# Kernel tuning notes

Hardware: AMD Instinct MI355X
Metric: run time of the kernel (lower is better)

The kernel has to match this reference:

```python
import jax, jax.numpy as jnp
import numpy as np

D_IN, D_MODEL = 512, 256
B, N = 2, 512


def setup_inputs() -> dict:
    key = jax.random.key(0)
    ks = jax.random.split(key, 8)
    xav_x = float(np.sqrt(2.0 / (D_IN + D_MODEL)))
    xav_p = float(np.sqrt(2.0 / (4 + D_MODEL)))
    return {
        "x": jax.random.normal(ks[0], (B, N, D_IN), dtype=jnp.float32),
        "pos": jax.random.normal(ks[1], (B, N, 4), dtype=jnp.float32),
        "attn_mask": jax.random.randint(ks[2], (B, N, N), 0, 2, dtype=jnp.int32),
        "Wx": jax.random.normal(ks[3], (D_IN, D_MODEL), dtype=jnp.float32) * xav_x,
        "bx": jnp.zeros((D_MODEL,), dtype=jnp.float32),
        "Wp": jax.random.normal(ks[4], (4, D_MODEL), dtype=jnp.float32) * xav_p,
        "bp": jnp.zeros((D_MODEL,), dtype=jnp.float32),
        "w": jax.random.normal(ks[5], (D_MODEL,), dtype=jnp.float32) * 0.05,
    }


def reference(x, pos, attn_mask, Wx, bx, Wp, bp, w):
    # projected, activated inputs: [B, N, d_model]
    h = jnp.tanh(x @ Wx + bx)
    # pairwise relative positions: [B, N, N, 4]
    rel = pos[:, :, None, :] - pos[:, None, :, :]
    # position MLP + tanh: [B, N, N, d_model]
    z = jnp.tanh(rel @ Wp + bp)
    # scores via dot with weight vector: [B, N, N]
    attn = jnp.einsum("bijd,d->bij", z, w)
    mask = attn_mask != 0
    attn = jnp.where(mask, attn, -jnp.inf)
    attn = jax.nn.softmax(attn, axis=2)
    attn = jnp.where(mask, attn, 0.0)
    # dropout is identity in eval mode
    # weighted sum: [B, N, d_model]
    output = jnp.einsum("bij,bjd->bid", attn, h)
    return (output, attn)
```

## Files before the change

kernel.cpp:

```cpp
#include <hip/hip_runtime.h>
#include <hip/hip_bf16.h>
#include <math.h>

#define BATCH   2
#define SEQ     512
#define DIN     512
#define DM      256

#define LOG2E2  2.88539008177792681f

#if __has_builtin(__builtin_amdgcn_exp2f)
#define EXP2(x) __builtin_amdgcn_exp2f(x)
#else
#define EXP2(x) exp2f(x)
#endif
#if __has_builtin(__builtin_amdgcn_rcpf)
#define RCP(x) __builtin_amdgcn_rcpf(x)
#else
#define RCP(x) (1.0f / (x))
#endif

__device__ __forceinline__ float tanh_from_scaled(float targ) {
    return fmaf(-2.0f, RCP(1.0f + EXP2(targ)), 1.0f);
}

__global__ __launch_bounds__(512) void produce_k(
    const float* __restrict__ pos,
    const float* __restrict__ Wp,
    const float* __restrict__ x,
    const float* __restrict__ Wx,
    const float* __restrict__ bx,
    float* __restrict__ EBf,
    float* __restrict__ h)
{
    const int tid = threadIdx.x;

    if (blockIdx.x < 128) {
        const int b  = blockIdx.x >> 6;
        const int q  = blockIdx.x & 63;
        const int d0 = 4 * q;
        const float4 p = ((const float4*)pos)[b * SEQ + tid];
        #pragma unroll
        for (int i = 0; i < 4; i++) {
            const int d = d0 + i;
            const float P = fmaf(p.x, Wp[d], fmaf(p.y, Wp[DM + d],
                            fmaf(p.z, Wp[2*DM + d], p.w * Wp[3*DM + d])));
            EBf[((size_t)(b * DM + d)) * SEQ + tid] = EXP2(-LOG2E2 * P);
        }
        return;
    }

    __shared__ float  s_xt[2][32][68];
    __shared__ float  s_wt[2][64][32];
    __shared__ float4 s_part[256];

    const int idx = blockIdx.x - 128;
    const int rt  = idx >> 3;
    const int ct  = idx & 7;
    const int kh  = __builtin_amdgcn_readfirstlane(tid >> 8);
    const int t   = tid & 255;
    const int ty  = t >> 3;
    const int tx  = t & 7;
    const int row = rt * 32 + ty;

    float4 acc = make_float4(0.f, 0.f, 0.f, 0.f);

    for (int ks = 0; ks < 4; ks++) {
        const int k0 = kh * 256 + ks * 64;
        #pragma unroll
        for (int s = 0; s < 2; s++) {
            const int fidx = t * 2 + s;
            const int r = fidx >> 4, c = fidx & 15;
            *(float4*)&s_xt[kh][r][4 * c] =
                *(const float4*)(x + (size_t)(rt * 32 + r) * DIN + k0 + 4 * c);
        }
        #pragma unroll
        for (int s = 0; s < 2; s++) {
            const int fidx = t * 2 + s;
            const int r = fidx >> 3, c = fidx & 7;
            *(float4*)&s_wt[kh][r][4 * c] =
                *(const float4*)(Wx + (size_t)(k0 + r) * DM + ct * 32 + 4 * c);
        }
        __syncthreads();

        #pragma unroll 8
        for (int k = 0; k < 64; k++) {
            const float  xv = s_xt[kh][ty][k];
            const float4 wq = *(const float4*)&s_wt[kh][k][4 * tx];
            acc.x = fmaf(xv, wq.x, acc.x);
            acc.y = fmaf(xv, wq.y, acc.y);
            acc.z = fmaf(xv, wq.z, acc.z);
            acc.w = fmaf(xv, wq.w, acc.w);
        }
        __syncthreads();
    }

    if (kh == 1) s_part[t] = acc;
    __syncthreads();
    if (kh == 0) {
        const float4 q4 = s_part[t];
        const float4 bq = *(const float4*)(bx + ct * 32 + 4 * tx);
        float4 o;
        o.x = tanh_from_scaled(LOG2E2 * (acc.x + q4.x + bq.x));
        o.y = tanh_from_scaled(LOG2E2 * (acc.y + q4.y + bq.y));
        o.z = tanh_from_scaled(LOG2E2 * (acc.z + q4.z + bq.z));
        o.w = tanh_from_scaled(LOG2E2 * (acc.w + q4.w + bq.w));
        *(float4*)(h + (size_t)row * DM + ct * 32 + 4 * tx) = o;
    }
}

__global__ __launch_bounds__(512) void attend_k(
    const float* __restrict__ pos,
    const float* __restrict__ Wp,
    const float* __restrict__ bp,
    const int*   __restrict__ mask,
    const float* __restrict__ wv,
    const float* __restrict__ EBf,
    const float* __restrict__ h,
    float* __restrict__ out,
    float* __restrict__ attn_out)
{
    const int b   = blockIdx.x >> 7;
    const int i0  = (blockIdx.x & 127) * 4;
    const int tid = threadIdx.x;
    const int l   = tid & 63;

    __shared__ float4 s_ea[DM];
    __shared__ float  s_p[4][SEQ];
    __shared__ float  s_red[4][8];
    __shared__ float  s_o[7][4][DM];

    {
        const int d  = tid & 255;
        const int rp = __builtin_amdgcn_readfirstlane(tid >> 8);
        const int r0 = rp * 2;
        const float4 p0 = ((const float4*)pos)[b * SEQ + i0 + r0];
        const float4 p1 = ((const float4*)pos)[b * SEQ + i0 + r0 + 1];
        const float wp0 = Wp[d], wp1 = Wp[DM + d], wp2 = Wp[2*DM + d], wp3 = Wp[3*DM + d];
        const float bpd = bp[d];
        const float P0 = fmaf(p0.x, wp0, fmaf(p0.y, wp1, fmaf(p0.z, wp2, p0.w * wp3)));
        const float P1 = fmaf(p1.x, wp0, fmaf(p1.y, wp1, fmaf(p1.z, wp2, p1.w * wp3)));
        float* se = (float*)&s_ea[d];
        se[r0]     = EXP2(LOG2E2 * (P0 + bpd));
        se[r0 + 1] = EXP2(LOG2E2 * (P1 + bpd));
    }
    __syncthreads();

    const float* __restrict__ EBj = EBf + (size_t)b * DM * SEQ + tid;

    float a0 = 0.f, a1 = 0.f, a2 = 0.f, a3 = 0.f;
    #pragma unroll 8
    for (int t = 0; t < 128; t++) {
        const float eb0 = EBj[(size_t)(2*t) * SEQ];
        const float eb1 = EBj[(size_t)(2*t + 1) * SEQ];
        const float4 eA = s_ea[2*t];
        const float4 eB = s_ea[2*t + 1];
        const float w0 = wv[2*t];
        const float w1 = wv[2*t + 1];

        {
            const float y0 = fmaf(eA.x, eb0, 1.f), y1 = fmaf(eB.x, eb1, 1.f);
            a0 = fmaf(fmaf(w0, y1, w1 * y0), RCP(y0 * y1), a0);
        }
        {
            const float y0 = fmaf(eA.y, eb0, 1.f), y1 = fmaf(eB.y, eb1, 1.f);
            a1 = fmaf(fmaf(w0, y1, w1 * y0), RCP(y0 * y1), a1);
        }
        {
            const float y0 = fmaf(eA.z, eb0, 1.f), y1 = fmaf(eB.z, eb1, 1.f);
            a2 = fmaf(fmaf(w0, y1, w1 * y0), RCP(y0 * y1), a2);
        }
        {
            const float y0 = fmaf(eA.w, eb0, 1.f), y1 = fmaf(eB.w, eb1, 1.f);
            a3 = fmaf(fmaf(w0, y1, w1 * y0), RCP(y0 * y1), a3);
        }
    }

    const size_t mrow = (size_t)b * SEQ * SEQ + (size_t)i0 * SEQ + tid;
    const int m0 = mask[mrow];
    const int m1 = mask[mrow + SEQ];
    const int m2 = mask[mrow + 2*SEQ];
    const int m3 = mask[mrow + 3*SEQ];
    float p0 = m0 ? EXP2(-LOG2E2 * a0) : 0.f;
    float p1 = m1 ? EXP2(-LOG2E2 * a1) : 0.f;
    float p2 = m2 ? EXP2(-LOG2E2 * a2) : 0.f;
    float p3 = m3 ? EXP2(-LOG2E2 * a3) : 0.f;

    float s0 = p0, s1 = p1, s2 = p2, s3 = p3;
    #pragma unroll
    for (int off = 32; off; off >>= 1) {
        s0 += __shfl_xor(s0, off, 64);
        s1 += __shfl_xor(s1, off, 64);
        s2 += __shfl_xor(s2, off, 64);
        s3 += __shfl_xor(s3, off, 64);
    }
    const int w = tid >> 6;
    if (l == 0) { s_red[0][w] = s0; s_red[1][w] = s1; s_red[2][w] = s2; s_red[3][w] = s3; }
    __syncthreads();

    {
        const float4 r0a = ((const float4*)s_red[0])[0], r0b = ((const float4*)s_red[0])[1];
        const float4 r1a = ((const float4*)s_red[1])[0], r1b = ((const float4*)s_red[1])[1];
        const float4 r2a = ((const float4*)s_red[2])[0], r2b = ((const float4*)s_red[2])[1];
        const float4 r3a = ((const float4*)s_red[3])[0], r3b = ((const float4*)s_red[3])[1];
        p0 *= __fdividef(1.0f, (r0a.x+r0a.y+r0a.z+r0a.w) + (r0b.x+r0b.y+r0b.z+r0b.w));
        p1 *= __fdividef(1.0f, (r1a.x+r1a.y+r1a.z+r1a.w) + (r1b.x+r1b.y+r1b.z+r1b.w));
        p2 *= __fdividef(1.0f, (r2a.x+r2a.y+r2a.z+r2a.w) + (r2b.x+r2b.y+r2b.z+r2b.w));
        p3 *= __fdividef(1.0f, (r3a.x+r3a.y+r3a.z+r3a.w) + (r3b.x+r3b.y+r3b.z+r3b.w));
    }

    attn_out[mrow]         = p0;
    attn_out[mrow + SEQ]   = p1;
    attn_out[mrow + 2*SEQ] = p2;
    attn_out[mrow + 3*SEQ] = p3;
    s_p[0][tid] = p0; s_p[1][tid] = p1; s_p[2][tid] = p2; s_p[3][tid] = p3;
    __syncthreads();

    const int dq = tid & 63;
    const int js = __builtin_amdgcn_readfirstlane(tid >> 6);
    const float* __restrict__ hp = h + (size_t)(b * SEQ + js * 64) * DM + 4 * dq;
    const float* __restrict__ q0p = &s_p[0][js * 64];
    const float* __restrict__ q1p = &s_p[1][js * 64];
    const float* __restrict__ q2p = &s_p[2][js * 64];
    const float* __restrict__ q3p = &s_p[3][js * 64];

    float4 a0v = make_float4(0,0,0,0), a1v = a0v, a2v = a0v, a3v = a0v;
    #pragma unroll 4
    for (int jj = 0; jj < 16; jj++) {
        const float4 P0 = *(const float4*)(q0p + 4 * jj);
        const float4 P1 = *(const float4*)(q1p + 4 * jj);
        const float4 P2 = *(const float4*)(q2p + 4 * jj);
        const float4 P3 = *(const float4*)(q3p + 4 * jj);
        const float4 h0 = *(const float4*)(hp + (size_t)(4*jj + 0) * DM);
        const float4 h1 = *(const float4*)(hp + (size_t)(4*jj + 1) * DM);
        const float4 h2 = *(const float4*)(hp + (size_t)(4*jj + 2) * DM);
        const float4 h3 = *(const float4*)(hp + (size_t)(4*jj + 3) * DM);

        a0v.x = fmaf(P0.x,h0.x,fmaf(P0.y,h1.x,fmaf(P0.z,h2.x,fmaf(P0.w,h3.x,a0v.x))));
        a0v.y = fmaf(P0.x,h0.y,fmaf(P0.y,h1.y,fmaf(P0.z,h2.y,fmaf(P0.w,h3.y,a0v.y))));
        a0v.z = fmaf(P0.x,h0.z,fmaf(P0.y,h1.z,fmaf(P0.z,h2.z,fmaf(P0.w,h3.z,a0v.z))));
        a0v.w = fmaf(P0.x,h0.w,fmaf(P0.y,h1.w,fmaf(P0.z,h2.w,fmaf(P0.w,h3.w,a0v.w))));
        a1v.x = fmaf(P1.x,h0.x,fmaf(P1.y,h1.x,fmaf(P1.z,h2.x,fmaf(P1.w,h3.x,a1v.x))));
        a1v.y = fmaf(P1.x,h0.y,fmaf(P1.y,h1.y,fmaf(P1.z,h2.y,fmaf(P1.w,h3.y,a1v.y))));
        a1v.z = fmaf(P1.x,h0.z,fmaf(P1.y,h1.z,fmaf(P1.z,h2.z,fmaf(P1.w,h3.z,a1v.z))));
        a1v.w = fmaf(P1.x,h0.w,fmaf(P1.y,h1.w,fmaf(P1.z,h2.w,fmaf(P1.w,h3.w,a1v.w))));
        a2v.x = fmaf(P2.x,h0.x,fmaf(P2.y,h1.x,fmaf(P2.z,h2.x,fmaf(P2.w,h3.x,a2v.x))));
        a2v.y = fmaf(P2.x,h0.y,fmaf(P2.y,h1.y,fmaf(P2.z,h2.y,fmaf(P2.w,h3.y,a2v.y))));
        a2v.z = fmaf(P2.x,h0.z,fmaf(P2.y,h1.z,fmaf(P2.z,h2.z,fmaf(P2.w,h3.z,a2v.z))));
        a2v.w = fmaf(P2.x,h0.w,fmaf(P2.y,h1.w,fmaf(P2.z,h2.w,fmaf(P2.w,h3.w,a2v.w))));
        a3v.x = fmaf(P3.x,h0.x,fmaf(P3.y,h1.x,fmaf(P3.z,h2.x,fmaf(P3.w,h3.x,a3v.x))));
        a3v.y = fmaf(P3.x,h0.y,fmaf(P3.y,h1.y,fmaf(P3.z,h2.y,fmaf(P3.w,h3.y,a3v.y))));
        a3v.z = fmaf(P3.x,h0.z,fmaf(P3.y,h1.z,fmaf(P3.z,h2.z,fmaf(P3.w,h3.z,a3v.z))));
        a3v.w = fmaf(P3.x,h0.w,fmaf(P3.y,h1.w,fmaf(P3.z,h2.w,fmaf(P3.w,h3.w,a3v.w))));
    }

    if (js > 0) {
        *(float4*)&s_o[js - 1][0][4 * dq] = a0v;
        *(float4*)&s_o[js - 1][1][4 * dq] = a1v;
        *(float4*)&s_o[js - 1][2][4 * dq] = a2v;
        *(float4*)&s_o[js - 1][3][4 * dq] = a3v;
    }
    __syncthreads();
    if (js == 0) {
        #pragma unroll
        for (int s = 0; s < 7; s++) {
            const float4 q0 = *(const float4*)&s_o[s][0][4 * dq];
            const float4 q1 = *(const float4*)&s_o[s][1][4 * dq];
            const float4 q2 = *(const float4*)&s_o[s][2][4 * dq];
            const float4 q3 = *(const float4*)&s_o[s][3][4 * dq];
            a0v.x += q0.x; a0v.y += q0.y; a0v.z += q0.z; a0v.w += q0.w;
            a1v.x += q1.x; a1v.y += q1.y; a1v.z += q1.z; a1v.w += q1.w;
            a2v.x += q2.x; a2v.y += q2.y; a2v.z += q2.z; a2v.w += q2.w;
            a3v.x += q3.x; a3v.y += q3.y; a3v.z += q3.z; a3v.w += q3.w;
        }
        float* __restrict__ op = out + (size_t)(b * SEQ + i0) * DM + 4 * dq;
        *(float4*)(op)        = a0v;
        *(float4*)(op + DM)   = a1v;
        *(float4*)(op + 2*DM) = a2v;
        *(float4*)(op + 3*DM) = a3v;
    }
}

extern "C" void kernel_launch(void* const* d_in, const int* in_sizes, int n_in,
                              void* d_out, int out_size, void* d_ws, size_t ws_size,
                              hipStream_t stream) {
    const float* x    = (const float*)d_in[0];
    const float* pos  = (const float*)d_in[1];
    const int*   mask = (const int*)  d_in[2];
    const float* Wx   = (const float*)d_in[3];
    const float* bx   = (const float*)d_in[4];
    const float* Wp   = (const float*)d_in[5];
    const float* bp   = (const float*)d_in[6];
    const float* wv   = (const float*)d_in[7];

    float* out      = (float*)d_out;
    float* attn_out = (float*)d_out + (size_t)BATCH*SEQ*DM;

    char*  ws  = (char*)d_ws;
    float* h   = (float*)(ws);
    float* EBf = (float*)(ws + (size_t)BATCH*SEQ*DM*4);

    produce_k<<<384, 512, 0, stream>>>(pos, Wp, x, Wx, bx, EBf, h);
    attend_k <<<(BATCH*SEQ)/4, 512, 0, stream>>>(pos, Wp, bp, mask, wv, EBf, h, out, attn_out);
}
```

Measured before the change: 107.8 us.

## Interleave EB table as float4 over d and fuse EB production into GEMM blocks

Result: faster. 99.15 us (-8.1%).

```diff
diff --git a/kernel.cpp b/kernel.cpp
--- a/kernel.cpp
+++ b/kernel.cpp
@@ -6,6 +6,7 @@
 #define SEQ     512
 #define DIN     512
 #define DM      256
+#define DM4     (DM/4)
 
 #define LOG2E2  2.88539008177792681f
 
@@ -30,31 +31,45 @@
     const float* __restrict__ x,
     const float* __restrict__ Wx,
     const float* __restrict__ bx,
-    float* __restrict__ EBf,
+    float4* __restrict__ EB4,
     float* __restrict__ h)
 {
     const int tid = threadIdx.x;
-
-    if (blockIdx.x < 128) {
-        const int b  = blockIdx.x >> 6;
-        const int q  = blockIdx.x & 63;
-        const int d0 = 4 * q;
+    const int idx = blockIdx.x;
+
+    if (idx < 128) {
+        const int b  = idx >> 6;
+        const int d4 = idx & 63;
+        const int d0 = 4 * d4;
         const float4 p = ((const float4*)pos)[b * SEQ + tid];
-        #pragma unroll
-        for (int i = 0; i < 4; i++) {
-            const int d = d0 + i;
-            const float P = fmaf(p.x, Wp[d], fmaf(p.y, Wp[DM + d],
-                            fmaf(p.z, Wp[2*DM + d], p.w * Wp[3*DM + d])));
-            EBf[((size_t)(b * DM + d)) * SEQ + tid] = EXP2(-LOG2E2 * P);
-        }
-        return;
+        float4 e;
+        {
+            const float P = fmaf(p.x, Wp[d0], fmaf(p.y, Wp[DM + d0],
+                            fmaf(p.z, Wp[2*DM + d0], p.w * Wp[3*DM + d0])));
+            e.x = EXP2(-LOG2E2 * P);
+        }
+        {
+            const float P = fmaf(p.x, Wp[d0+1], fmaf(p.y, Wp[DM + d0+1],
+                            fmaf(p.z, Wp[2*DM + d0+1], p.w * Wp[3*DM + d0+1])));
+            e.y = EXP2(-LOG2E2 * P);
+        }
+        {
+            const float P = fmaf(p.x, Wp[d0+2], fmaf(p.y, Wp[DM + d0+2],
+                            fmaf(p.z, Wp[2*DM + d0+2], p.w * Wp[3*DM + d0+2])));
+            e.z = EXP2(-LOG2E2 * P);
+        }
+        {
+            const float P = fmaf(p.x, Wp[d0+3], fmaf(p.y, Wp[DM + d0+3],
+                            fmaf(p.z, Wp[2*DM + d0+3], p.w * Wp[3*DM + d0+3])));
+            e.w = EXP2(-LOG2E2 * P);
+        }
+        EB4[((size_t)(b * DM4 + d4)) * SEQ + tid] = e;
     }
 
     __shared__ float  s_xt[2][32][68];
     __shared__ float  s_wt[2][64][32];
     __shared__ float4 s_part[256];
 
-    const int idx = blockIdx.x - 128;
     const int rt  = idx >> 3;
     const int ct  = idx & 7;
     const int kh  = __builtin_amdgcn_readfirstlane(tid >> 8);
@@ -115,7 +130,7 @@
     const float* __restrict__ bp,
     const int*   __restrict__ mask,
     const float* __restrict__ wv,
-    const float* __restrict__ EBf,
+    const float4* __restrict__ EB4,
     const float* __restrict__ h,
     float* __restrict__ out,
     float* __restrict__ attn_out)
@@ -146,41 +161,39 @@
     }
     __syncthreads();
 
-    const float* __restrict__ EBj = EBf + (size_t)b * DM * SEQ + tid;
-
-    float a0 = 0.f, a1 = 0.f, a2 = 0.f, a3 = 0.f;
-    #pragma unroll 8
-    for (int t = 0; t < 128; t++) {
-        const float eb0 = EBj[(size_t)(2*t) * SEQ];
-        const float eb1 = EBj[(size_t)(2*t + 1) * SEQ];
-        const float4 eA = s_ea[2*t];
-        const float4 eB = s_ea[2*t + 1];
-        const float w0 = wv[2*t];
-        const float w1 = wv[2*t + 1];
-
-        {
-            const float y0 = fmaf(eA.x, eb0, 1.f), y1 = fmaf(eB.x, eb1, 1.f);
-            a0 = fmaf(fmaf(w0, y1, w1 * y0), RCP(y0 * y1), a0);
-        }
-        {
-            const float y0 = fmaf(eA.y, eb0, 1.f), y1 = fmaf(eB.y, eb1, 1.f);
-            a1 = fmaf(fmaf(w0, y1, w1 * y0), RCP(y0 * y1), a1);
-        }
-        {
-            const float y0 = fmaf(eA.z, eb0, 1.f), y1 = fmaf(eB.z, eb1, 1.f);
-            a2 = fmaf(fmaf(w0, y1, w1 * y0), RCP(y0 * y1), a2);
-        }
-        {
-            const float y0 = fmaf(eA.w, eb0, 1.f), y1 = fmaf(eB.w, eb1, 1.f);
-            a3 = fmaf(fmaf(w0, y1, w1 * y0), RCP(y0 * y1), a3);
-        }
-    }
-
     const size_t mrow = (size_t)b * SEQ * SEQ + (size_t)i0 * SEQ + tid;
     const int m0 = mask[mrow];
     const int m1 = mask[mrow + SEQ];
     const int m2 = mask[mrow + 2*SEQ];
     const int m3 = mask[mrow + 3*SEQ];
+
+    const float4* __restrict__ EBj = EB4 + (size_t)b * DM4 * SEQ + tid;
+
+    float a0 = 0.f, a1 = 0.f, a2 = 0.f, a3 = 0.f;
+    #pragma unroll 4
+    for (int t = 0; t < DM4; t++) {
+        const float4 eb = EBj[(size_t)t * SEQ];
+        const float4 e0 = s_ea[4*t + 0];
+        const float4 e1 = s_ea[4*t + 1];
+        const float4 e2 = s_ea[4*t + 2];
+        const float4 e3 = s_ea[4*t + 3];
+        const float4 w4 = *(const float4*)(wv + 4*t);
+
+#define SCORE_ROW(acc, C) { \
+        const float y0 = fmaf(e0.C, eb.x, 1.f); \
+        const float y1 = fmaf(e1.C, eb.y, 1.f); \
+        const float y2 = fmaf(e2.C, eb.z, 1.f); \
+        const float y3 = fmaf(e3.C, eb.w, 1.f); \
+        acc = fmaf(fmaf(w4.x, y1, w4.y * y0), RCP(y0 * y1), acc); \
+        acc = fmaf(fmaf(w4.z, y3, w4.w * y2), RCP(y2 * y3), acc); \
+    }
+        SCORE_ROW(a0, x)
+        SCORE_ROW(a1, y)
+        SCORE_ROW(a2, z)
+        SCORE_ROW(a3, w)
+#undef SCORE_ROW
+    }
+
     float p0 = m0 ? EXP2(-LOG2E2 * a0) : 0.f;
     float p1 = m1 ? EXP2(-LOG2E2 * a1) : 0.f;
     float p2 = m2 ? EXP2(-LOG2E2 * a2) : 0.f;
@@ -300,6 +313,7 @@
     float* h   = (float*)(ws);
     float* EBf = (float*)(ws + (size_t)BATCH*SEQ*DM*4);
 
-    produce_k<<<384, 512, 0, stream>>>(pos, Wp, x, Wx, bx, EBf, h);
-    attend_k <<<(BATCH*SEQ)/4, 512, 0, stream>>>(pos, Wp, bp, mask, wv, EBf, h, out, attn_out);
+    produce_k<<<256, 512, 0, stream>>>(pos, Wp, x, Wx, bx, (float4*)EBf, h);
+    attend_k <<<(BATCH*SEQ)/4, 512, 0, stream>>>(pos, Wp, bp, mask, wv,
+                                                 (const float4*)EBf, h, out, attn_out);
 }
```
